# Kernel optimization log

Hardware: AMD Instinct MI355X
Metric: run time of the kernel (lower is better)

Reference implementation:

```python
import jax, jax.numpy as jnp
import numpy as np

KERNEL = 5
STRIDE = 1
DN = ('NHWC', 'HWIO', 'NHWC')
PRIOR_VAR = 0.01


def setup_inputs() -> dict:
    key = jax.random.key(0)
    k1, k2, k3 = jax.random.split(key, 3)
    mu_in = jax.random.normal(k1, (32, 224, 224, 3), dtype=jnp.float32)
    # GlorotNormal-ish scale for a 5x5x3 -> 64 kernel
    w_mu = jax.random.normal(k2, (5, 5, 3, 64), dtype=jnp.float32) * 0.12
    # original init: uniform in [min_sigma, ini_sigma] = [-4.6, -2.25]
    w_sigma = jax.random.uniform(k3, (64,), dtype=jnp.float32, minval=-4.6, maxval=-2.25)
    return {"mu_in": mu_in, "w_mu": w_mu, "w_sigma": w_sigma}


def reference(mu_in, w_mu, w_sigma):
    # KL regularizer: broadcast of (64,) logvar against (5,5,3,64) mu, mean over all
    kl = 0.5 * jnp.mean(
        jnp.log(PRIOR_VAR) - 1.0 - w_sigma
        + jax.nn.softplus(w_sigma) / PRIOR_VAR
        + jnp.square(w_mu) / PRIOR_VAR
    )

    w_sigma_2 = jax.nn.softplus(w_sigma)  # log(1+exp(w_sigma))

    # Mean path: standard conv2d, VALID, stride 1, NHWC
    mu_out = jax.lax.conv_general_dilated(
        mu_in, w_mu, (STRIDE, STRIDE), 'VALID', dimension_numbers=DN
    )  # [B, Ho, Wo, K]

    # Variance path: per-output-location sum over the k*k*C patch of x^2 / x_dim.
    # Same math as the original extract_patches + reduce_sum, but computed as a
    # channel-summed box filter on x^2 (no im2col materialization).
    C = mu_in.shape[-1]
    x_dim = jnp.asarray(KERNEL * KERNEL * C, mu_in.dtype)
    ones_k = jnp.ones((KERNEL, KERNEL, C, 1), mu_in.dtype)
    sq = jax.lax.conv_general_dilated(
        jnp.square(mu_in), ones_k, (STRIDE, STRIDE), 'VALID', dimension_numbers=DN
    ) / x_dim  # [B, Ho, Wo, 1]

    Sigma_out = jax.nn.softplus(w_sigma_2 * sq)  # broadcast -> [B, Ho, Wo, K]
    return (mu_out, Sigma_out, kl)
```

## Files before the change

### kernel.cpp

```cpp
#include <hip/hip_runtime.h>
#include <math.h>

#define BATCH 32
#define HIN   224
#define WIN   224
#define CIN   3
#define KOUT  64
#define RK    5
#define HOUT  220
#define WOUT  220

#define TS       16
#define PATCH    20
#define NTOT ((size_t)BATCH * HOUT * WOUT * KOUT)

typedef float  v4f    __attribute__((ext_vector_type(4)));
typedef short  short8 __attribute__((ext_vector_type(8)));

#define WS_WF_FRAGS 768
#define WS_WSG_OFF  12288

__device__ __forceinline__ float exp2_hw(float x) { float r; asm("v_exp_f32 %0, %1" : "=v"(r) : "v"(x)); return r; }
__device__ __forceinline__ float log2_hw(float x) { float r; asm("v_log_f32 %0, %1" : "=v"(r) : "v"(x)); return r; }
#define LOG2E 1.44269504088896f
#define LN2   0.69314718055995f

__device__ __forceinline__ float softplus_hw(float x) {
    float t = exp2_hw(-fabsf(x) * LOG2E);
    return fmaxf(x, 0.0f) + LN2 * log2_hw(1.0f + t);
}
__device__ __forceinline__ float softplus_pos(float y) {
    return y + LN2 * log2_hw(1.0f + exp2_hw(-y * LOG2E));
}
__device__ __forceinline__ short f2bf(float x) {
    unsigned u = __float_as_uint(x);
    u = (u + 0x7FFFu + ((u >> 16) & 1u)) >> 16;
    return (short)u;
}

__global__ __launch_bounds__(256) void vdp_prep_kernel(
    const float* __restrict__ w_mu, const float* __restrict__ w_sigma,
    void* __restrict__ ws, float* __restrict__ out)
{
    __shared__ float red[4];
    short8* wf = (short8*)ws;
    float* wsg = (float*)((char*)ws + WS_WSG_OFF);
    const int t = threadIdx.x;
    const int blk = blockIdx.x;

    if (blk < 3) {
        const int f = blk * 256 + t;
        const int s  = f >> 8;
        const int nb = (f >> 6) & 3;
        const int l  = f & 63;
        const int ch = nb * 16 + (l & 15);
        const int h2 = l >> 4;
        short8 r;
        #pragma unroll
        for (int i = 0; i < 8; ++i) {
            const int k = s * 32 + h2 * 8 + i;
            const int kh = k >> 4, inner = k & 15;
            float v = 0.0f;
            if (inner < 15 && k < 80) {
                const int kw = inner / 3;
                const int c  = inner - kw * 3;
                v = w_mu[((kh * 5 + kw) * 3 + c) * KOUT + ch];
            }
            r[i] = f2bf(v);
        }
        wf[f] = r;
        return;
    }

    if (t < KOUT) wsg[t] = softplus_hw(w_sigma[t]);

    float s = 0.0f;
    for (int i = t; i < RK * RK * CIN * KOUT; i += 256) {
        const float v = w_mu[i];
        s = fmaf(v, v, s);
    }
    float u = s * (100.0f / 4800.0f);
    if (t < KOUT) {
        const float wsv = w_sigma[t];
        u += (-wsv + softplus_hw(wsv) * 100.0f) * (1.0f / 64.0f);
    }
    #pragma unroll
    for (int off = 32; off > 0; off >>= 1)
        u += __shfl_down(u, off, 64);
    if ((t & 63) == 0) red[t >> 6] = u;
    __syncthreads();
    if (t == 0) {
        const float U = red[0] + red[1] + red[2] + red[3];
        out[2 * NTOT] = 0.5f * (-4.6051701860f - 1.0f + U);
    }
}

__global__ __launch_bounds__(256, 4) void vdp_conv_kernel(
    const float* __restrict__ mu_in, const void* __restrict__ ws, float* __restrict__ out)
{
    __shared__ float s_row[PATCH * 64];
    __shared__ float s_ssq[PATCH][PATCH];

    const int tid  = threadIdx.x;
    const int lane = tid & 63;
    const int wid  = tid >> 6;
    const int p    = lane & 15;
    const int h2   = lane >> 4;

    const int b = blockIdx.z;
    int ho0 = blockIdx.y * TS; if (ho0 > HOUT - TS) ho0 = HOUT - TS;
    int wo0 = blockIdx.x * TS; if (wo0 > WOUT - TS) wo0 = WOUT - TS;

    const short8* wfg = (const short8*)ws;
    short8 wf[12];
    #pragma unroll
    for (int f = 0; f < 12; ++f) wf[f] = wfg[f * 64 + lane];
    const float* wsg_g = (const float*)((const char*)ws + WS_WSG_OFF);
    const v4f wsg_kg = *(const v4f*)(wsg_g + p * 4);

    {
        const float* gb = mu_in + ((size_t)b * HIN + ho0) * (WIN * CIN) + wo0 * CIN;
        #pragma unroll
        for (int it = 0; it < 2; ++it) {
            const int ci = it * 256 + (tid & ~63);
            if (ci < 320) {
                const int il = ci + (tid & 63);
                const int r  = il >> 4;
                int cc = il & 15; if (cc > 14) cc = 14;
                const float* g = gb + r * (WIN * CIN) + cc * 4;
                __builtin_amdgcn_global_load_lds(
                    (const __attribute__((address_space(1))) void*)g,
                    (__attribute__((address_space(3))) void*)(s_row + ci * 4),
                    16, 0, 0);
            }
        }
    }
    asm volatile("s_waitcnt vmcnt(0) lgkmcnt(0)" ::: "memory");
    __builtin_amdgcn_s_barrier();

    for (int idx = tid; idx < PATCH * PATCH; idx += 256) {
        const int r = idx / PATCH;
        const int px = idx - r * PATCH;
        const float x0 = s_row[r * 64 + 3 * px], x1 = s_row[r * 64 + 3 * px + 1],
                    x2 = s_row[r * 64 + 3 * px + 2];
        s_ssq[r][px] = fmaf(x0, x0, fmaf(x1, x1, x2 * x2));
    }
    asm volatile("s_waitcnt lgkmcnt(0)" ::: "memory");
    __builtin_amdgcn_s_barrier();

    #pragma unroll 1
    for (int j = 0; j < 4; ++j) {
        const int rt = (wid << 2) | j;
        const size_t rowbase = (((size_t)b * HOUT + ho0 + rt) * WOUT + wo0) * KOUT;

        short8 pf[3];
        #pragma unroll
        for (int s = 0; s < 3; ++s) {
            int ridx = rt + 2 * s + (h2 >> 1);
            ridx = ridx > PATCH - 1 ? PATCH - 1 : ridx;
            const float* rp = s_row + ridx * 64 + 3 * p + 8 * (h2 & 1);
            union { unsigned u[4]; short8 v; } cv;
            asm("v_cvt_pk_bf16_f32 %0, %1, %2" : "=v"(cv.u[0]) : "v"(rp[0]), "v"(rp[1]));
            asm("v_cvt_pk_bf16_f32 %0, %1, %2" : "=v"(cv.u[1]) : "v"(rp[2]), "v"(rp[3]));
            asm("v_cvt_pk_bf16_f32 %0, %1, %2" : "=v"(cv.u[2]) : "v"(rp[4]), "v"(rp[5]));
            asm("v_cvt_pk_bf16_f32 %0, %1, %2" : "=v"(cv.u[3]) : "v"(rp[6]), "v"(rp[7]));
            pf[s] = cv.v;
        }

        v4f acc[4];
        #pragma unroll
        for (int nb = 0; nb < 4; ++nb) {
            v4f a = {0.0f, 0.0f, 0.0f, 0.0f};
            #pragma unroll
            for (int s = 0; s < 3; ++s)
                a = __builtin_amdgcn_mfma_f32_16x16x32_bf16(wf[s * 4 + nb], pf[s], a, 0, 0, 0);
            acc[nb] = a;
        }

        float* mp = out + rowbase + (size_t)p * KOUT + h2 * 4;
        #pragma unroll
        for (int nb = 0; nb < 4; ++nb)
            *(v4f*)(mp + nb * 16) = acc[nb];

        float sqv = 0.0f;
        if (lane < 16) {
            #pragma unroll
            for (int kh = 0; kh < RK; ++kh)
                #pragma unroll
                for (int kw = 0; kw < RK; ++kw)
                    sqv += s_ssq[rt + kh][p + kw];
            sqv *= (1.0f / 75.0f);
        }
        float* sp = out + NTOT + rowbase + p * 4;
        #pragma unroll
        for (int pp = 0; pp < 4; ++pp) {
            const int px = (h2 << 2) | pp;
            const float sq = __shfl(sqv, px, 64);
            v4f sg;
            sg.x = softplus_pos(wsg_kg.x * sq);
            sg.y = softplus_pos(wsg_kg.y * sq);
            sg.z = softplus_pos(wsg_kg.z * sq);
            sg.w = softplus_pos(wsg_kg.w * sq);
            *(v4f*)(sp + (size_t)px * KOUT) = sg;
        }
    }
}

extern "C" void kernel_launch(void* const* d_in, const int* in_sizes, int n_in,
                              void* d_out, int out_size, void* d_ws, size_t ws_size,
                              hipStream_t stream)
{
    (void)in_sizes; (void)n_in; (void)ws_size; (void)out_size;
    const float* mu_in   = (const float*)d_in[0];
    const float* w_mu    = (const float*)d_in[1];
    const float* w_sigma = (const float*)d_in[2];
    float* out = (float*)d_out;

    vdp_prep_kernel<<<4, 256, 0, stream>>>(w_mu, w_sigma, d_ws, out);
    dim3 grid((WOUT + TS - 1) / TS, (HOUT + TS - 1) / TS, BATCH);
    vdp_conv_kernel<<<grid, 256, 0, stream>>>(mu_in, d_ws, out);
}
```

Baseline: 172.0 us.

## Make conv kernel persistent with double-buffered LDS tile prefetch

Replaces the one-block-per-tile grid with 896 persistent blocks that each handle 7 consecutive tiles, with an XCD-aware block-to-work remapping. The next tile's input patch is prefetched into a second LDS buffer via global_load_lds while the current tile's MFMA and softplus stores run. The goal is to hide input load latency and amortise weight-fragment loads across tiles. In exchange it doubles staging LDS, adds per-tile barriers, and relies on a hand-set vmcnt(32) wait that must match the number of outstanding memory operations.

```diff
diff --git a/kernel.cpp b/kernel.cpp
--- a/kernel.cpp
+++ b/kernel.cpp
@@ -12,6 +12,9 @@
 
 #define TS       16
 #define PATCH    20
+#define NT_TILES (14 * 14 * BATCH)
+#define NBLK     896
+#define TPB      7
 #define NTOT ((size_t)BATCH * HOUT * WOUT * KOUT)
 
 typedef float  v4f    __attribute__((ext_vector_type(4)));
@@ -95,10 +98,34 @@
     }
 }
 
+__device__ __forceinline__ void stage_tile(const float* __restrict__ mu_in, int t,
+                                           float* buf, int tid)
+{
+    const int b  = t / 196;
+    const int r2 = t - b * 196;
+    int ho0 = (r2 / 14) * TS; if (ho0 > HOUT - TS) ho0 = HOUT - TS;
+    int wo0 = (r2 % 14) * TS; if (wo0 > WOUT - TS) wo0 = WOUT - TS;
+    const float* gb = mu_in + ((size_t)b * HIN + ho0) * (WIN * CIN) + wo0 * CIN;
+    #pragma unroll
+    for (int it = 0; it < 2; ++it) {
+        const int ci = it * 256 + (tid & ~63);
+        if (ci < 320) {
+            const int il = ci + (tid & 63);
+            const int r  = il >> 4;
+            int cc = il & 15; if (cc > 14) cc = 14;
+            const float* g = gb + r * (WIN * CIN) + cc * 4;
+            __builtin_amdgcn_global_load_lds(
+                (const __attribute__((address_space(1))) void*)g,
+                (__attribute__((address_space(3))) void*)(buf + ci * 4),
+                16, 0, 0);
+        }
+    }
+}
+
 __global__ __launch_bounds__(256, 4) void vdp_conv_kernel(
     const float* __restrict__ mu_in, const void* __restrict__ ws, float* __restrict__ out)
 {
-    __shared__ float s_row[PATCH * 64];
+    __shared__ float s_row[2][PATCH * 64];
     __shared__ float s_ssq[PATCH][PATCH];
 
     const int tid  = threadIdx.x;
@@ -107,9 +134,9 @@
     const int p    = lane & 15;
     const int h2   = lane >> 4;
 
-    const int b = blockIdx.z;
-    int ho0 = blockIdx.y * TS; if (ho0 > HOUT - TS) ho0 = HOUT - TS;
-    int wo0 = blockIdx.x * TS; if (wo0 > WOUT - TS) wo0 = WOUT - TS;
+    const int bid = blockIdx.x;
+    const int wg  = (bid & 7) * (NBLK / 8) + (bid >> 3);
+    const int t0  = wg * TPB;
 
     const short8* wfg = (const short8*)ws;
     short8 wf[12];
@@ -118,91 +145,99 @@
     const float* wsg_g = (const float*)((const char*)ws + WS_WSG_OFF);
     const v4f wsg_kg = *(const v4f*)(wsg_g + p * 4);
 
-    {
-        const float* gb = mu_in + ((size_t)b * HIN + ho0) * (WIN * CIN) + wo0 * CIN;
-        #pragma unroll
-        for (int it = 0; it < 2; ++it) {
-            const int ci = it * 256 + (tid & ~63);
-            if (ci < 320) {
-                const int il = ci + (tid & 63);
-                const int r  = il >> 4;
-                int cc = il & 15; if (cc > 14) cc = 14;
-                const float* g = gb + r * (WIN * CIN) + cc * 4;
-                __builtin_amdgcn_global_load_lds(
-                    (const __attribute__((address_space(1))) void*)g,
-                    (__attribute__((address_space(3))) void*)(s_row + ci * 4),
-                    16, 0, 0);
-            }
-        }
-    }
+    stage_tile(mu_in, t0, s_row[0], tid);
     asm volatile("s_waitcnt vmcnt(0) lgkmcnt(0)" ::: "memory");
     __builtin_amdgcn_s_barrier();
 
-    for (int idx = tid; idx < PATCH * PATCH; idx += 256) {
-        const int r = idx / PATCH;
-        const int px = idx - r * PATCH;
-        const float x0 = s_row[r * 64 + 3 * px], x1 = s_row[r * 64 + 3 * px + 1],
-                    x2 = s_row[r * 64 + 3 * px + 2];
-        s_ssq[r][px] = fmaf(x0, x0, fmaf(x1, x1, x2 * x2));
-    }
-    asm volatile("s_waitcnt lgkmcnt(0)" ::: "memory");
-    __builtin_amdgcn_s_barrier();
-
+    int cur = 0;
     #pragma unroll 1
-    for (int j = 0; j < 4; ++j) {
-        const int rt = (wid << 2) | j;
-        const size_t rowbase = (((size_t)b * HOUT + ho0 + rt) * WOUT + wo0) * KOUT;
-
-        short8 pf[3];
-        #pragma unroll
-        for (int s = 0; s < 3; ++s) {
-            int ridx = rt + 2 * s + (h2 >> 1);
-            ridx = ridx > PATCH - 1 ? PATCH - 1 : ridx;
-            const float* rp = s_row + ridx * 64 + 3 * p + 8 * (h2 & 1);
-            union { unsigned u[4]; short8 v; } cv;
-            asm("v_cvt_pk_bf16_f32 %0, %1, %2" : "=v"(cv.u[0]) : "v"(rp[0]), "v"(rp[1]));
-            asm("v_cvt_pk_bf16_f32 %0, %1, %2" : "=v"(cv.u[1]) : "v"(rp[2]), "v"(rp[3]));
-            asm("v_cvt_pk_bf16_f32 %0, %1, %2" : "=v"(cv.u[2]) : "v"(rp[4]), "v"(rp[5]));
-            asm("v_cvt_pk_bf16_f32 %0, %1, %2" : "=v"(cv.u[3]) : "v"(rp[6]), "v"(rp[7]));
-            pf[s] = cv.v;
-        }
-
-        v4f acc[4];
-        #pragma unroll
-        for (int nb = 0; nb < 4; ++nb) {
-            v4f a = {0.0f, 0.0f, 0.0f, 0.0f};
-            #pragma unroll
-            for (int s = 0; s < 3; ++s)
-                a = __builtin_amdgcn_mfma_f32_16x16x32_bf16(wf[s * 4 + nb], pf[s], a, 0, 0, 0);
-            acc[nb] = a;
-        }
-
-        float* mp = out + rowbase + (size_t)p * KOUT + h2 * 4;
-        #pragma unroll
-        for (int nb = 0; nb < 4; ++nb)
-            *(v4f*)(mp + nb * 16) = acc[nb];
-
-        float sqv = 0.0f;
-        if (lane < 16) {
-            #pragma unroll
-            for (int kh = 0; kh < RK; ++kh)
+    for (int k = 0; k < TPB; ++k) {
+        const int t = t0 + k;
+
+        if (k > 0) {
+            asm volatile("s_waitcnt vmcnt(32) lgkmcnt(0)" ::: "memory");
+            __builtin_amdgcn_s_barrier();
+            __builtin_amdgcn_sched_barrier(0);
+        }
+
+        const float* srow = s_row[cur];
+
+        for (int idx = tid; idx < PATCH * PATCH; idx += 256) {
+            const int r = idx / PATCH;
+            const int px = idx - r * PATCH;
+            const float x0 = srow[r * 64 + 3 * px], x1 = srow[r * 64 + 3 * px + 1],
+                        x2 = srow[r * 64 + 3 * px + 2];
+            s_ssq[r][px] = fmaf(x0, x0, fmaf(x1, x1, x2 * x2));
+        }
+        asm volatile("s_waitcnt lgkmcnt(0)" ::: "memory");
+        __builtin_amdgcn_s_barrier();
+
+        if (k < TPB - 1) stage_tile(mu_in, t + 1, s_row[cur ^ 1], tid);
+        __builtin_amdgcn_sched_barrier(0);
+
+        const int b  = t / 196;
+        const int r2 = t - b * 196;
+        int ho0 = (r2 / 14) * TS; if (ho0 > HOUT - TS) ho0 = HOUT - TS;
+        int wo0 = (r2 % 14) * TS; if (wo0 > WOUT - TS) wo0 = WOUT - TS;
+
+        #pragma unroll 1
+        for (int j = 0; j < 4; ++j) {
+            const int rt = (wid << 2) | j;
+            const size_t rowbase = (((size_t)b * HOUT + ho0 + rt) * WOUT + wo0) * KOUT;
+
+            short8 pf[3];
+            #pragma unroll
+            for (int s = 0; s < 3; ++s) {
+                int ridx = rt + 2 * s + (h2 >> 1);
+                ridx = ridx > PATCH - 1 ? PATCH - 1 : ridx;
+                const float* rp = srow + ridx * 64 + 3 * p + 8 * (h2 & 1);
+                union { unsigned u[4]; short8 v; } cv;
+                asm("v_cvt_pk_bf16_f32 %0, %1, %2" : "=v"(cv.u[0]) : "v"(rp[0]), "v"(rp[1]));
+                asm("v_cvt_pk_bf16_f32 %0, %1, %2" : "=v"(cv.u[1]) : "v"(rp[2]), "v"(rp[3]));
+                asm("v_cvt_pk_bf16_f32 %0, %1, %2" : "=v"(cv.u[2]) : "v"(rp[4]), "v"(rp[5]));
+                asm("v_cvt_pk_bf16_f32 %0, %1, %2" : "=v"(cv.u[3]) : "v"(rp[6]), "v"(rp[7]));
+                pf[s] = cv.v;
+            }
+
+            v4f acc[4];
+            #pragma unroll
+            for (int nb = 0; nb < 4; ++nb) {
+                v4f a = {0.0f, 0.0f, 0.0f, 0.0f};
                 #pragma unroll
-                for (int kw = 0; kw < RK; ++kw)
-                    sqv += s_ssq[rt + kh][p + kw];
-            sqv *= (1.0f / 75.0f);
-        }
-        float* sp = out + NTOT + rowbase + p * 4;
-        #pragma unroll
-        for (int pp = 0; pp < 4; ++pp) {
-            const int px = (h2 << 2) | pp;
-            const float sq = __shfl(sqv, px, 64);
-            v4f sg;
-            sg.x = softplus_pos(wsg_kg.x * sq);
-            sg.y = softplus_pos(wsg_kg.y * sq);
-            sg.z = softplus_pos(wsg_kg.z * sq);
-            sg.w = softplus_pos(wsg_kg.w * sq);
-            *(v4f*)(sp + (size_t)px * KOUT) = sg;
-        }
+                for (int s = 0; s < 3; ++s)
+                    a = __builtin_amdgcn_mfma_f32_16x16x32_bf16(wf[s * 4 + nb], pf[s], a, 0, 0, 0);
+                acc[nb] = a;
+            }
+
+            float* mp = out + rowbase + (size_t)p * KOUT + h2 * 4;
+            #pragma unroll
+            for (int nb = 0; nb < 4; ++nb)
+                *(v4f*)(mp + nb * 16) = acc[nb];
+
+            float sqv = 0.0f;
+            if (lane < 16) {
+                #pragma unroll
+                for (int kh = 0; kh < RK; ++kh)
+                    #pragma unroll
+                    for (int kw = 0; kw < RK; ++kw)
+                        sqv += s_ssq[rt + kh][p + kw];
+                sqv *= (1.0f / 75.0f);
+            }
+            float* sp = out + NTOT + rowbase + p * 4;
+            #pragma unroll
+            for (int pp = 0; pp < 4; ++pp) {
+                const int px = (h2 << 2) | pp;
+                const float sq = __shfl(sqv, px, 64);
+                v4f sg;
+                sg.x = softplus_pos(wsg_kg.x * sq);
+                sg.y = softplus_pos(wsg_kg.y * sq);
+                sg.z = softplus_pos(wsg_kg.z * sq);
+                sg.w = softplus_pos(wsg_kg.w * sq);
+                *(v4f*)(sp + (size_t)px * KOUT) = sg;
+            }
+        }
+
+        cur ^= 1;
     }
 }
 
@@ -217,6 +252,5 @@
     float* out = (float*)d_out;
 
     vdp_prep_kernel<<<4, 256, 0, stream>>>(w_mu, w_sigma, d_ws, out);
-    dim3 grid((WOUT + TS - 1) / TS, (HOUT + TS - 1) / TS, BATCH);
-    vdp_conv_kernel<<<grid, 256, 0, stream>>>(mu_in, d_ws, out);
-}
+    vdp_conv_kernel<<<NBLK, 256, 0, stream>>>(mu_in, d_ws, out);
+}
```

Result: slower. 194.3 us (+13.0%).
